# Kernel optimization log

Measured on AMD Instinct MI355X. Metric: run time of the kernel, lower is better.

## Reference

```python
import jax, jax.numpy as jnp
import numpy as np

# Model constants (hard-coded in the torch module / xLSTM config)
B, T, D, H, V = 512, 128, 128, 4, 30000
HD = D // H          # head dim = 32
K = 4                # causal conv1d kernel size
UP = 192             # gated FFN up dim: round_up(1.3*128, 64)
NB = 2               # num sLSTM blocks
EPS = 1e-5


def layernorm(x, w):
    mu = x.mean(-1, keepdims=True)
    var = x.var(-1, keepdims=True)
    return (x - mu) * jax.lax.rsqrt(var + EPS) * w


def setup_inputs() -> dict:
    key = jax.random.key(0)
    ks = iter(jax.random.split(key, 32))

    def rn(shape, s=0.05):
        return jax.random.normal(next(ks), shape, jnp.float32) * s

    tokens = jax.random.randint(next(ks), (B, T), 0, V)
    return {
        "tokens": tokens,
        "emb": rn((V, D), 0.02),
        "ln1_w": jnp.ones((NB, D)),
        "conv_w": rn((NB, D, K), 0.1),          # depthwise causal conv weights
        "conv_b": jnp.zeros((NB, D)),
        "Wi": rn((NB, H, HD, HD), 0.1),          # headwise gate projections
        "Wf": rn((NB, H, HD, HD), 0.1),
        "Wz": rn((NB, H, HD, HD), 0.1),
        "Wo": rn((NB, H, HD, HD), 0.1),
        "Rk": rn((NB, H, HD, 4 * HD), 0.1),      # per-head recurrent kernel
        "cell_b": jnp.zeros((NB, H, 4 * HD)),
        "gn_w": jnp.ones((NB, D)),               # multi-head (group) norm weight
        "ln2_w": jnp.ones((NB, D)),
        "ff_w1": rn((NB, D, 2 * UP), 0.05),      # gated FFN up proj
        "ff_b1": jnp.zeros((NB, 2 * UP)),
        "ff_w2": rn((NB, UP, D), 0.05),
        "ff_b2": jnp.zeros((NB, D)),
        "post_norm_w": jnp.ones((D,)),
        "cls_w1": rn((D, 64), 0.05),
        "cls_b1": jnp.zeros((64,)),
        "cls_w2": rn((64, 2), 0.05),
        "cls_b2": jnp.zeros((2,)),
    }


def slstm_layer(x, conv_w, conv_b, Wi, Wf, Wz, Wo, Rk, cell_b, gn_w):
    # x: [B,T,D]. Causal depthwise conv (left pad K-1) + swish.
    xp = jnp.pad(x, ((0, 0), (K - 1, 0), (0, 0)))
    conv = conv_b + sum(xp[:, k:k + T, :] * conv_w[:, k] for k in range(K))
    x_conv = jax.nn.silu(conv)
    xc = x_conv.reshape(B, T, H, HD)
    xh = x.reshape(B, T, H, HD)
    # i/f gates read the conv branch, z/o gates read x (xLSTM sLSTMLayer).
    i_in = jnp.einsum('bthd,hde->bthe', xc, Wi)
    f_in = jnp.einsum('bthd,hde->bthe', xc, Wf)
    z_in = jnp.einsum('bthd,hde->bthe', xh, Wz)
    o_in = jnp.einsum('bthd,hde->bthe', xh, Wo)
    gates = jnp.concatenate([i_in, f_in, z_in, o_in], -1)  # [B,T,H,4HD]
    gates = jnp.swapaxes(gates, 0, 1)                       # [T,B,H,4HD]

    def step(carry, g_t):
        h, c, n, m = carry  # each [B,H,HD]
        raw = g_t + jnp.einsum('bhd,hdg->bhg', h, Rk) + cell_b
        ir, fr, zr, og = jnp.split(raw, 4, axis=-1)
        # exponential gating with stabilizer state m
        m_new = jnp.maximum(fr + m, ir)
        ig = jnp.exp(ir - m_new)
        fg = jnp.exp(fr + m - m_new)
        c_new = fg * c + ig * jnp.tanh(zr)
        n_new = fg * n + ig
        h_new = jax.nn.sigmoid(og) * c_new / n_new
        return (h_new, c_new, n_new, m_new), h_new

    z0 = jnp.zeros((B, H, HD), x.dtype)
    _, ys = jax.lax.scan(step, (z0, z0, z0, z0), gates)
    y = jnp.swapaxes(ys, 0, 1)  # [B,T,H,HD]
    # multi-head layernorm (group norm over each head)
    mu = y.mean(-1, keepdims=True)
    var = y.var(-1, keepdims=True)
    yn = (y - mu) * jax.lax.rsqrt(var + EPS)
    return yn.reshape(B, T, D) * gn_w


def reference(tokens, emb, ln1_w, conv_w, conv_b, Wi, Wf, Wz, Wo, Rk, cell_b,
              gn_w, ln2_w, ff_w1, ff_b1, ff_w2, ff_b2, post_norm_w,
              cls_w1, cls_b1, cls_w2, cls_b2):
    x = emb[tokens]  # [B,T,D]
    for b in range(NB):
        x = x + slstm_layer(layernorm(x, ln1_w[b]), conv_w[b], conv_b[b],
                            Wi[b], Wf[b], Wz[b], Wo[b], Rk[b], cell_b[b], gn_w[b])
        h = layernorm(x, ln2_w[b]) @ ff_w1[b] + ff_b1[b]
        gate, up = jnp.split(h, 2, axis=-1)
        x = x + (jax.nn.gelu(gate) * up) @ ff_w2[b] + ff_b2[b]
    x = layernorm(x, post_norm_w)
    pooled = x.mean(axis=1)  # [B,D]
    h1 = jax.nn.relu(pooled @ cls_w1 + cls_b1)
    return h1 @ cls_w2 + cls_b2  # [B,2] logits
```

## Files before the change

### kernel.cpp

```cpp
#include <hip/hip_runtime.h>

typedef unsigned short u16;
typedef unsigned int u32;
typedef __attribute__((ext_vector_type(8))) short short8;
typedef __attribute__((ext_vector_type(4))) short s16x4;
typedef __attribute__((ext_vector_type(4))) float f32x4;
typedef __attribute__((ext_vector_type(2))) float f32x2;
typedef __attribute__((ext_vector_type(2))) int i32x2;

#define BB 512
#define TT 128
#define DD 128
#define HH 4
#define NBB 2
#define BT (BB*TT)
#define EPSF 1e-5f
#define LOG2E 1.4426950408889634f

__device__ __forceinline__ float bf2f(u16 u){ return __uint_as_float(((u32)u) << 16); }
__device__ __forceinline__ u16 f2bf(float f){
  u32 x = __float_as_uint(f);
  u32 r = x + 0x7fffu + ((x >> 16) & 1u);
  return (u16)(r >> 16);
}
__device__ __forceinline__ float bcastf(float v, int lane){
  return __uint_as_float(__builtin_amdgcn_readlane(__float_as_uint(v), lane));
}
__device__ __forceinline__ float gelu_fast(float x){
  float u = 0.7978845608028654f * (x + 0.044715f * x * x * x);
  float e2 = __builtin_amdgcn_exp2f(2.f * LOG2E * u);
  return x - x * __builtin_amdgcn_rcpf(e2 + 1.f);
}
#define DPP_ADD(v, ctrl, rmask, bc) \
  v += __int_as_float(__builtin_amdgcn_update_dpp(0, __float_as_int(v), (ctrl), (rmask), 0xf, (bc)))
__device__ __forceinline__ float wsum64(float v){
  DPP_ADD(v, 0x111, 0xf, true);
  DPP_ADD(v, 0x112, 0xf, true);
  DPP_ADD(v, 0x114, 0xf, true);
  DPP_ADD(v, 0x118, 0xf, true);
  DPP_ADD(v, 0x142, 0xa, false);
  DPP_ADD(v, 0x143, 0xc, false);
  return bcastf(v, 63);
}
__device__ __forceinline__ float rsum_rows01(float v){
  DPP_ADD(v, 0x111, 0xf, true);
  DPP_ADD(v, 0x112, 0xf, true);
  DPP_ADD(v, 0x114, 0xf, true);
  DPP_ADD(v, 0x118, 0xf, true);
  DPP_ADD(v, 0x142, 0xa, false);
  return v;
}
__device__ __forceinline__ float down32(float v){
  i32x2 r = __builtin_amdgcn_permlane32_swap(__float_as_int(v), __float_as_int(v), false, false);
  return __int_as_float(r.y);
}

__global__ __launch_bounds__(256) void k_convert(
    const float* __restrict__ ff_w1, const float* __restrict__ ff_w2,
    const float* __restrict__ Wi, const float* __restrict__ Wf,
    const float* __restrict__ Wz, const float* __restrict__ Wo,
    u16* __restrict__ w1T, u16* __restrict__ w2T,
    u16* __restrict__ gifT, u16* __restrict__ gzoT){
  int tid = blockIdx.x * 256 + threadIdx.x;
  const int n1 = NBB*384*128;
  if (tid < n1){
    int nb = tid / (384*128); int r = tid - nb*384*128; int n = r >> 7, k = r & 127;
    w1T[tid] = f2bf(ff_w1[(nb*128 + k)*384 + n]); return;
  }
  tid -= n1;
  const int n2 = NBB*128*192;
  if (tid < n2){
    int nb = tid / (128*192); int r = tid - nb*128*192; int n = r / 192, k = r - n*192;
    w2T[tid] = f2bf(ff_w2[(nb*192 + k)*128 + n]); return;
  }
  tid -= n2;
  const int n3 = NBB*HH*64*32;
  if (tid < n3){
    int nb = tid / (HH*64*32); int r = tid - nb*HH*64*32;
    int h = r >> 11; int r2 = r & 2047; int n = r2 >> 5, k = r2 & 31;
    const float* W = (n < 32) ? Wi : Wf; int nn = n & 31;
    gifT[tid] = f2bf(W[((nb*HH + h)*32 + k)*32 + nn]); return;
  }
  tid -= n3;
  if (tid < n3){
    int nb = tid / (HH*64*32); int r = tid - nb*HH*64*32;
    int h = r >> 11; int r2 = r & 2047; int n = r2 >> 5, k = r2 & 31;
    const float* W = (n < 32) ? Wz : Wo; int nn = n & 31;
    gzoT[tid] = f2bf(W[((nb*HH + h)*32 + k)*32 + nn]); return;
  }
}

__global__ __launch_bounds__(256) void k_lnconv(float* __restrict__ x,
    const int* __restrict__ tok, const float* __restrict__ emb,
    const float* __restrict__ ln1_w, const float* __restrict__ conv_w,
    const float* __restrict__ conv_b, u16* __restrict__ xn_bf,
    u16* __restrict__ xc_bf, int nb, int useemb){
  __shared__ float lnbuf[35][128];
  int b = blockIdx.x >> 2, tile = blockIdx.x & 3;
  int t0 = tile * 32;
  int wid = threadIdx.x >> 6, l = threadIdx.x & 63;
  for (int tt = wid; tt < 35; tt += 4){
    int t = t0 - 3 + tt;
    if (t < 0){
      lnbuf[tt][2*l] = 0.f; lnbuf[tt][2*l+1] = 0.f;
    } else {
      const float* src = useemb ? (emb + (size_t)tok[b*TT + t]*128)
                                : (x + (size_t)(b*TT + t)*128);
      float2 v = ((const float2*)src)[l];
      float s  = wsum64(v.x + v.y);
      float sq = wsum64(v.x*v.x + v.y*v.y);
      float mu = s * (1.f/128.f);
      float var = sq * (1.f/128.f) - mu*mu;
      float rs = rsqrtf(var + EPSF);
      float2 w = ((const float2*)(ln1_w + nb*128))[l];
      float y0 = (v.x - mu)*rs*w.x, y1 = (v.y - mu)*rs*w.y;
      lnbuf[tt][2*l] = y0; lnbuf[tt][2*l+1] = y1;
      if (tt >= 3){
        u32 pk = (u32)f2bf(y0) | ((u32)f2bf(y1) << 16);
        ((u32*)(xn_bf + (size_t)(b*TT + t)*128))[l] = pk;
        if (useemb) ((float2*)(x + (size_t)(b*TT + t)*128))[l] = v;
      }
    }
  }
  __syncthreads();
  for (int e = threadIdx.x; e < 32*128; e += 256){
    int tt = e >> 7, d = e & 127;
    float s = conv_b[nb*128 + d];
    #pragma unroll
    for (int k = 0; k < 4; k++)
      s += lnbuf[tt + k][d] * conv_w[(nb*128 + d)*4 + k];
    float sig = 1.f / (1.f + __expf(-s));
    xc_bf[(size_t)(b*TT + t0 + tt)*128 + d] = f2bf(s * sig);
  }
}

__global__ __launch_bounds__(256) void k_gates(const u16* __restrict__ xc_bf,
    const u16* __restrict__ xn_bf, const u16* __restrict__ gifT,
    const u16* __restrict__ gzoT, u16* __restrict__ gates, int nb){
  int m0 = blockIdx.x * 64;
  int b = m0 >> 7;
  int t00 = m0 & 127;
  int h = threadIdx.x >> 6, l = threadIdx.x & 63;
  short8 bfr[2][4];
  {
    const u16* B0 = gifT + (size_t)(nb*HH + h)*64*32;
    const u16* B1 = gzoT + (size_t)(nb*HH + h)*64*32;
    #pragma unroll
    for (int jt = 0; jt < 4; jt++){
      bfr[0][jt] = *(const short8*)(B0 + (jt*16 + (l & 15))*32 + (l >> 4)*8);
      bfr[1][jt] = *(const short8*)(B1 + (jt*16 + (l & 15))*32 + (l >> 4)*8);
    }
  }
  u16* gb = gates + (size_t)(b*HH + h)*TT*128;
  #pragma unroll
  for (int z = 0; z < 2; z++){
    const u16* A = z ? xn_bf : xc_bf;
    #pragma unroll
    for (int rg = 0; rg < 4; rg++){
      int r0 = m0 + rg*16;
      short8 a = *(const short8*)(A + (size_t)(r0 + (l & 15))*128 + h*32 + (l >> 4)*8);
      int tt = t00 + rg*16 + (l >> 4)*4;
      #pragma unroll
      for (int jt = 0; jt < 4; jt++){
        f32x4 acc = {0.f, 0.f, 0.f, 0.f};
        acc = __builtin_amdgcn_mfma_f32_16x16x32_bf16(a, bfr[z][jt], acc, 0, 0, 0);
        int cloc = z*64 + jt*16 + (l & 15);
        s16x4 pk;
        #pragma unroll
        for (int r = 0; r < 4; r++) pk[r] = (short)f2bf(acc[r]);
        *(s16x4*)(gb + ((size_t)(tt >> 3)*128 + cloc)*8 + (tt & 7)) = pk;
      }
    }
  }
}

__global__ __launch_bounds__(256, 2) void k_scan(const u16* __restrict__ gates,
    const float* __restrict__ Rk, const float* __restrict__ cell_b,
    const float* __restrict__ gn_w, float* __restrict__ x,
    float* __restrict__ dump, int nb){
  int wid = threadIdx.x >> 6, l = threadIdx.x & 63;
  int pair = blockIdx.x * 4 + wid;
  int b = pair >> 2, h = pair & 3;
  f32x2 rk[32];
  const float* Rkh = Rk + (size_t)(nb*HH + h)*32*128;
  #pragma unroll
  for (int d = 0; d < 32; d++){
    rk[d].x = Rkh[d*128 + l];
    rk[d].y = Rkh[d*128 + l + 64];
  }
  f32x2 cb = { cell_b[(nb*HH + h)*128 + l], cell_b[(nb*HH + h)*128 + l + 64] };
  int e = l & 31;
  bool lo = (l < 32);
  float gnw = gn_w[nb*128 + h*32 + e];
  float hs = 0.f, cs = 0.f, ns = 0.f, ms = 0.f;
  const u16* gbase = gates + (size_t)(b*HH + h)*TT*128;
  float* xp = lo ? (x + (size_t)(b*TT)*128 + h*32 + e) : (dump + pair*32 + e);
  int xstr = lo ? 128 : 0;
  float xnext = xp[0];
  short8 ga = *(const short8*)(gbase + (size_t)l*8);
  short8 gb = *(const short8*)(gbase + (size_t)(l + 64)*8);
  for (int t8 = 0; t8 < 16; t8++){
    short8 na  = *(const short8*)(gbase + ((size_t)(t8+1)*128 + l)*8);
    short8 nb2 = *(const short8*)(gbase + ((size_t)(t8+1)*128 + l + 64)*8);
    #pragma unroll
    for (int k = 0; k < 8; k++){
      float xcur = xnext;
      xnext = xp[xstr];
      f32x2 acc0 = { bf2f((u16)ga[k]) + cb.x, bf2f((u16)gb[k]) + cb.y };
      f32x2 acc1 = {0.f, 0.f}, acc2 = {0.f, 0.f}, acc3 = {0.f, 0.f};
      #pragma unroll
      for (int d = 0; d < 32; d += 4){
        float h0 = bcastf(hs, d),   h1 = bcastf(hs, d+1);
        float h2 = bcastf(hs, d+2), h3 = bcastf(hs, d+3);
        acc0 = __builtin_elementwise_fma((f32x2){h0,h0}, rk[d],   acc0);
        acc1 = __builtin_elementwise_fma((f32x2){h1,h1}, rk[d+1], acc1);
        acc2 = __builtin_elementwise_fma((f32x2){h2,h2}, rk[d+2], acc2);
        acc3 = __builtin_elementwise_fma((f32x2){h3,h3}, rk[d+3], acc3);
      }
      f32x2 rr = (acc0 + acc1) + (acc2 + acc3);
      float r0 = rr.x, r1 = rr.y;
      float fx = down32(r0);
      float ox = down32(r1);
      float mnew = fmaxf(fx + ms, r0);
      float ig = __builtin_amdgcn_exp2f((r0 - mnew) * LOG2E);
      float fg = __builtin_amdgcn_exp2f((fx + ms - mnew) * LOG2E);
      float e2 = __builtin_amdgcn_exp2f(2.f * LOG2E * r1);
      float th = fmaf(-2.f, __builtin_amdgcn_rcpf(e2 + 1.f), 1.f);
      cs = fmaf(fg, cs, ig * th);
      ns = fmaf(fg, ns, ig);
      ms = mnew;
      float se = __builtin_amdgcn_exp2f(-ox * LOG2E);
      hs = cs * __builtin_amdgcn_rcpf(fmaf(ns, se, ns));
      float s = rsum_rows01(hs);
      float sq = rsum_rows01(hs * hs);
      float mu = bcastf(s, 31) * (1.f/32.f);
      float var = bcastf(sq, 31) * (1.f/32.f) - mu*mu;
      float yn = (hs - mu) * __builtin_amdgcn_rsqf(var + EPSF) * gnw;
      xp[0] = xcur + yn;
      xp += xstr;
    }
    ga = na; gb = nb2;
  }
}

__global__ __launch_bounds__(512, 4) void k_ffn(float* __restrict__ x,
    const float* __restrict__ ln2_w, const u16* __restrict__ w1T,
    const float* __restrict__ ff_b1, const u16* __restrict__ w2T,
    const float* __restrict__ ff_b2, int nb){
  __shared__ u16 xln[64][136];
  __shared__ u16 hbuf[64][392];
  int m0 = blockIdx.x * 64;
  int w = threadIdx.x >> 6, l = threadIdx.x & 63;
  short8 w1f[3][4];
  const u16* W1 = w1T + (size_t)nb*384*128;
  #pragma unroll
  for (int j = 0; j < 3; j++)
    #pragma unroll
    for (int c = 0; c < 4; c++)
      w1f[j][c] = *(const short8*)(W1 + (size_t)((3*w + j)*16 + (l & 15))*128 + c*32 + (l >> 4)*8);
  short8 w2f[6];
  const u16* W2 = w2T + (size_t)nb*128*192;
  #pragma unroll
  for (int c = 0; c < 6; c++)
    w2f[c] = *(const short8*)(W2 + (size_t)(w*16 + (l & 15))*192 + c*32 + (l >> 4)*8);
  float2 lw = ((const float2*)(ln2_w + nb*128))[l];
  #pragma unroll
  for (int rr = 0; rr < 8; rr++){
    int row = w*8 + rr;
    float2 v = ((const float2*)(x + (size_t)(m0 + row)*128))[l];
    float s  = wsum64(v.x + v.y);
    float sq = wsum64(v.x*v.x + v.y*v.y);
    float mu = s * (1.f/128.f);
    float var = sq * (1.f/128.f) - mu*mu;
    float rs = rsqrtf(var + EPSF);
    ((u32*)xln[row])[l] = (u32)f2bf((v.x - mu)*rs*lw.x)
                        | ((u32)f2bf((v.y - mu)*rs*lw.y) << 16);
  }
  __syncthreads();
  #pragma unroll
  for (int rg = 0; rg < 4; rg++){
    short8 a[4];
    #pragma unroll
    for (int c = 0; c < 4; c++)
      a[c] = *(const short8*)(&xln[rg*16 + (l & 15)][c*32 + (l >> 4)*8]);
    #pragma unroll
    for (int j = 0; j < 3; j++){
      f32x4 acc = {0.f, 0.f, 0.f, 0.f};
      #pragma unroll
      for (int c = 0; c < 4; c++)
        acc = __builtin_amdgcn_mfma_f32_16x16x32_bf16(a[c], w1f[j][c], acc, 0, 0, 0);
      int col = (3*w + j)*16 + (l & 15);
      float bb = ff_b1[nb*384 + col];
      #pragma unroll
      for (int r = 0; r < 4; r++){
        int row = rg*16 + (l >> 4)*4 + r;
        hbuf[row][col] = f2bf(acc[r] + bb);
      }
    }
  }
  __syncthreads();
  {
    int row = threadIdx.x >> 3;
    int k0 = (threadIdx.x & 7) * 24;
    #pragma unroll
    for (int j2 = 0; j2 < 24; j2++){
      int k = k0 + j2;
      float g = bf2f(hbuf[row][k]);
      float u = bf2f(hbuf[row][k + 192]);
      hbuf[row][k] = f2bf(gelu_fast(g) * u);
    }
  }
  __syncthreads();
  #pragma unroll
  for (int rg = 0; rg < 4; rg++){
    f32x4 acc = {0.f, 0.f, 0.f, 0.f};
    #pragma unroll
    for (int c = 0; c < 6; c++){
      short8 a = *(const short8*)(&hbuf[rg*16 + (l & 15)][c*32 + (l >> 4)*8]);
      acc = __builtin_amdgcn_mfma_f32_16x16x32_bf16(a, w2f[c], acc, 0, 0, 0);
    }
    int col = w*16 + (l & 15);
    float bb = ff_b2[nb*128 + col];
    #pragma unroll
    for (int r = 0; r < 4; r++){
      int row = m0 + rg*16 + (l >> 4)*4 + r;
      x[(size_t)row*128 + col] += acc[r] + bb;
    }
  }
}

__global__ __launch_bounds__(256) void k_pool_cls(const float* __restrict__ x,
    const float* __restrict__ pw, const float* __restrict__ w1,
    const float* __restrict__ b1, const float* __restrict__ w2,
    const float* __restrict__ b2, float* __restrict__ out){
  __shared__ float red[4][128];
  __shared__ float pooled[128];
  __shared__ float h1s[64];
  int b = blockIdx.x;
  int wid = threadIdx.x >> 6, l = threadIdx.x & 63;
  float2 w = ((const float2*)pw)[l];
  float ax = 0.f, ay = 0.f;
  for (int t = wid; t < TT; t += 4){
    float2 v = ((const float2*)(x + (size_t)(b*TT + t)*128))[l];
    float s  = wsum64(v.x + v.y);
    float sq = wsum64(v.x*v.x + v.y*v.y);
    float mu = s * (1.f/128.f);
    float var = sq * (1.f/128.f) - mu*mu;
    float rs = rsqrtf(var + EPSF);
    ax += (v.x - mu)*rs*w.x;
    ay += (v.y - mu)*rs*w.y;
  }
  red[wid][2*l] = ax; red[wid][2*l+1] = ay;
  __syncthreads();
  if (threadIdx.x < 128){
    int d = threadIdx.x;
    pooled[d] = (red[0][d] + red[1][d] + red[2][d] + red[3][d]) * (1.f/128.f);
  }
  __syncthreads();
  if (threadIdx.x < 64){
    int j = threadIdx.x;
    float s = b1[j];
    for (int d = 0; d < 128; d++) s += pooled[d] * w1[d*64 + j];
    h1s[j] = fmaxf(s, 0.f);
  }
  __syncthreads();
  if (threadIdx.x < 2){
    int j = threadIdx.x;
    float s = b2[j];
    for (int k = 0; k < 64; k++) s += h1s[k] * w2[k*2 + j];
    out[b*2 + j] = s;
  }
}

extern "C" void kernel_launch(void* const* d_in, const int* in_sizes, int n_in,
                              void* d_out, int out_size, void* d_ws, size_t ws_size,
                              hipStream_t stream){
  const int*   tok    = (const int*)d_in[0];
  const float* emb    = (const float*)d_in[1];
  const float* ln1_w  = (const float*)d_in[2];
  const float* conv_w = (const float*)d_in[3];
  const float* conv_b = (const float*)d_in[4];
  const float* Wi     = (const float*)d_in[5];
  const float* Wf     = (const float*)d_in[6];
  const float* Wz     = (const float*)d_in[7];
  const float* Wo     = (const float*)d_in[8];
  const float* Rk     = (const float*)d_in[9];
  const float* cell_b = (const float*)d_in[10];
  const float* gn_w   = (const float*)d_in[11];
  const float* ln2_w  = (const float*)d_in[12];
  const float* ff_w1  = (const float*)d_in[13];
  const float* ff_b1  = (const float*)d_in[14];
  const float* ff_w2  = (const float*)d_in[15];
  const float* ff_b2  = (const float*)d_in[16];
  const float* postw  = (const float*)d_in[17];
  const float* cw1    = (const float*)d_in[18];
  const float* cb1    = (const float*)d_in[19];
  const float* cw2    = (const float*)d_in[20];
  const float* cb2    = (const float*)d_in[21];
  float* out = (float*)d_out;

  char* ws = (char*)d_ws;
  size_t off = 0;
  float* x      = (float*)(ws + off); off += (size_t)BT*128*4;
  u16*   xn_bf  = (u16*)(ws + off);   off += (size_t)BT*128*2;
  u16*   xc_bf  = (u16*)(ws + off);   off += (size_t)BT*128*2;
  u16*   gates  = (u16*)(ws + off);   off += (size_t)BT*512*2;
  u16*   w1T    = (u16*)(ws + off);   off += (size_t)NBB*384*128*2;
  u16*   w2T    = (u16*)(ws + off);   off += (size_t)NBB*128*192*2;
  u16*   gifT   = (u16*)(ws + off);   off += (size_t)NBB*HH*64*32*2;
  u16*   gzoT   = (u16*)(ws + off);   off += (size_t)NBB*HH*64*32*2;
  float* dump   = (float*)xn_bf;

  k_convert<<<704, 256, 0, stream>>>(ff_w1, ff_w2, Wi, Wf, Wz, Wo, w1T, w2T, gifT, gzoT);
  for (int nb = 0; nb < NBB; nb++){
    k_lnconv<<<BB*4, 256, 0, stream>>>(x, tok, emb, ln1_w, conv_w, conv_b,
                                       xn_bf, xc_bf, nb, nb == 0 ? 1 : 0);
    k_gates<<<BT/64, 256, 0, stream>>>(xc_bf, xn_bf, gifT, gzoT, gates, nb);
    k_scan<<<512, 256, 0, stream>>>(gates, Rk, cell_b, gn_w, x, dump, nb);
    k_ffn<<<BT/64, 512, 0, stream>>>(x, ln2_w, w1T, ff_b1, w2T, ff_b2, nb);
  }
  k_pool_cls<<<BB, 256, 0, stream>>>(x, postw, cw1, cb1, cw2, cb2, out);
}
```

Measured before the change: 304.4 us.

## Batch sLSTM recurrence across 16 sequences with split-bf16 MFMA

The scan kernel now has one wavefront per (16-sequence group, head). It computes the recurrent matvec for 16 batch rows at once with MFMA, using a hi/lo bf16 split of both Rk and h to approximate fp32 precision, instead of per-lane FMA over readlane broadcasts. The gates kernel writes gate preactivations with the cell bias folded in, in an MFMA-fragment layout. h is exchanged through LDS each step. The grid drops from 512 blocks of 256 threads to 128 single-wave blocks, which trades parallelism and latency hiding for far fewer instructions per step.

```diff
diff --git a/kernel.cpp b/kernel.cpp
--- a/kernel.cpp
+++ b/kernel.cpp
@@ -3,10 +3,8 @@
 typedef unsigned short u16;
 typedef unsigned int u32;
 typedef __attribute__((ext_vector_type(8))) short short8;
-typedef __attribute__((ext_vector_type(4))) short s16x4;
 typedef __attribute__((ext_vector_type(4))) float f32x4;
 typedef __attribute__((ext_vector_type(2))) float f32x2;
-typedef __attribute__((ext_vector_type(2))) int i32x2;
 
 #define BB 512
 #define TT 128
@@ -42,25 +40,14 @@
   DPP_ADD(v, 0x143, 0xc, false);
   return bcastf(v, 63);
 }
-__device__ __forceinline__ float rsum_rows01(float v){
-  DPP_ADD(v, 0x111, 0xf, true);
-  DPP_ADD(v, 0x112, 0xf, true);
-  DPP_ADD(v, 0x114, 0xf, true);
-  DPP_ADD(v, 0x118, 0xf, true);
-  DPP_ADD(v, 0x142, 0xa, false);
-  return v;
-}
-__device__ __forceinline__ float down32(float v){
-  i32x2 r = __builtin_amdgcn_permlane32_swap(__float_as_int(v), __float_as_int(v), false, false);
-  return __int_as_float(r.y);
-}
 
 __global__ __launch_bounds__(256) void k_convert(
     const float* __restrict__ ff_w1, const float* __restrict__ ff_w2,
     const float* __restrict__ Wi, const float* __restrict__ Wf,
     const float* __restrict__ Wz, const float* __restrict__ Wo,
+    const float* __restrict__ Rk,
     u16* __restrict__ w1T, u16* __restrict__ w2T,
-    u16* __restrict__ gifT, u16* __restrict__ gzoT){
+    u16* __restrict__ gifT, u16* __restrict__ gzoT, u16* __restrict__ rkf){
   int tid = blockIdx.x * 256 + threadIdx.x;
   const int n1 = NBB*384*128;
   if (tid < n1){
@@ -87,6 +74,20 @@
     int h = r >> 11; int r2 = r & 2047; int n = r2 >> 5, k = r2 & 31;
     const float* W = (n < 32) ? Wz : Wo; int nn = n & 31;
     gzoT[tid] = f2bf(W[((nb*HH + h)*32 + k)*32 + nn]); return;
+  }
+  tid -= n3;
+  const int n5 = NBB*HH*8*64*8;
+  if (tid < n5){
+    int j = tid & 7; int t2 = tid >> 3;
+    int l = t2 & 63; t2 >>= 6;
+    int m = t2 & 7; t2 >>= 3;
+    int h4 = t2 & 3; int nb = t2 >> 2;
+    float v = Rk[((size_t)((nb*HH + h4)*32) + (l >> 4)*8 + j)*128 + m*16 + (l & 15)];
+    u16 hi = f2bf(v);
+    u16 lo = f2bf(v - bf2f(hi));
+    size_t base = (((size_t)(nb*HH + h4)*8 + m)*64 + l)*16;
+    rkf[base + j] = hi;
+    rkf[base + 8 + j] = lo;
   }
 }
 
@@ -136,7 +137,8 @@
 
 __global__ __launch_bounds__(256) void k_gates(const u16* __restrict__ xc_bf,
     const u16* __restrict__ xn_bf, const u16* __restrict__ gifT,
-    const u16* __restrict__ gzoT, u16* __restrict__ gates, int nb){
+    const u16* __restrict__ gzoT, const float* __restrict__ cell_b,
+    u16* __restrict__ gfrag, int nb){
   int m0 = blockIdx.x * 64;
   int b = m0 >> 7;
   int t00 = m0 & 127;
@@ -151,7 +153,11 @@
       bfr[1][jt] = *(const short8*)(B1 + (jt*16 + (l & 15))*32 + (l >> 4)*8);
     }
   }
-  u16* gb = gates + (size_t)(b*HH + h)*TT*128;
+  u16* gf = gfrag + (size_t)((b >> 4)*4 + h)*TT*64*32;
+  int c = b & 15;
+  int gg = (l & 15) >> 2;
+  int r3 = l & 3;
+  const float* cbp = cell_b + (nb*HH + h)*128;
   #pragma unroll
   for (int z = 0; z < 2; z++){
     const u16* A = z ? xn_bf : xc_bf;
@@ -159,87 +165,137 @@
     for (int rg = 0; rg < 4; rg++){
       int r0 = m0 + rg*16;
       short8 a = *(const short8*)(A + (size_t)(r0 + (l & 15))*128 + h*32 + (l >> 4)*8);
-      int tt = t00 + rg*16 + (l >> 4)*4;
+      int tb = t00 + rg*16 + (l >> 4)*4;
       #pragma unroll
       for (int jt = 0; jt < 4; jt++){
         f32x4 acc = {0.f, 0.f, 0.f, 0.f};
         acc = __builtin_amdgcn_mfma_f32_16x16x32_bf16(a, bfr[z][jt], acc, 0, 0, 0);
         int cloc = z*64 + jt*16 + (l & 15);
-        s16x4 pk;
+        float cb = cbp[cloc];
+        int slot = (z*4 + jt)*4 + r3;
         #pragma unroll
-        for (int r = 0; r < 4; r++) pk[r] = (short)f2bf(acc[r]);
-        *(s16x4*)(gb + ((size_t)(tt >> 3)*128 + cloc)*8 + (tt & 7)) = pk;
+        for (int r = 0; r < 4; r++)
+          gf[((size_t)(tb + r)*64 + gg*16 + c)*32 + slot] = f2bf(acc[r] + cb);
       }
     }
   }
 }
 
-__global__ __launch_bounds__(256, 2) void k_scan(const u16* __restrict__ gates,
-    const float* __restrict__ Rk, const float* __restrict__ cell_b,
-    const float* __restrict__ gn_w, float* __restrict__ x,
-    float* __restrict__ dump, int nb){
-  int wid = threadIdx.x >> 6, l = threadIdx.x & 63;
-  int pair = blockIdx.x * 4 + wid;
-  int b = pair >> 2, h = pair & 3;
-  f32x2 rk[32];
-  const float* Rkh = Rk + (size_t)(nb*HH + h)*32*128;
-  #pragma unroll
-  for (int d = 0; d < 32; d++){
-    rk[d].x = Rkh[d*128 + l];
-    rk[d].y = Rkh[d*128 + l + 64];
-  }
-  f32x2 cb = { cell_b[(nb*HH + h)*128 + l], cell_b[(nb*HH + h)*128 + l + 64] };
-  int e = l & 31;
-  bool lo = (l < 32);
-  float gnw = gn_w[nb*128 + h*32 + e];
-  float hs = 0.f, cs = 0.f, ns = 0.f, ms = 0.f;
-  const u16* gbase = gates + (size_t)(b*HH + h)*TT*128;
-  float* xp = lo ? (x + (size_t)(b*TT)*128 + h*32 + e) : (dump + pair*32 + e);
-  int xstr = lo ? 128 : 0;
-  float xnext = xp[0];
-  short8 ga = *(const short8*)(gbase + (size_t)l*8);
-  short8 gb = *(const short8*)(gbase + (size_t)(l + 64)*8);
-  for (int t8 = 0; t8 < 16; t8++){
-    short8 na  = *(const short8*)(gbase + ((size_t)(t8+1)*128 + l)*8);
-    short8 nb2 = *(const short8*)(gbase + ((size_t)(t8+1)*128 + l + 64)*8);
-    #pragma unroll
-    for (int k = 0; k < 8; k++){
-      float xcur = xnext;
-      xnext = xp[xstr];
-      f32x2 acc0 = { bf2f((u16)ga[k]) + cb.x, bf2f((u16)gb[k]) + cb.y };
-      f32x2 acc1 = {0.f, 0.f}, acc2 = {0.f, 0.f}, acc3 = {0.f, 0.f};
+__global__ __launch_bounds__(64, 1) void k_scan(const u16* __restrict__ gfrag,
+    const u16* __restrict__ rkf, const float* __restrict__ gn_w,
+    float* __restrict__ x, int nb){
+  __shared__ u16 hb[2][16][40];
+  int l = threadIdx.x;
+  int g = blockIdx.x;
+  int hg = g & 3;
+  int c = l & 15, g2 = l >> 4;
+  int b = (g >> 2)*16 + c;
+  short8 afh[8], afl[8];
+  {
+    const u16* rk = rkf + (((size_t)(nb*HH + hg)*8)*64 + l)*16;
+    #pragma unroll
+    for (int m = 0; m < 8; m++){
+      afh[m] = *(const short8*)(rk + (size_t)m*64*16);
+      afl[m] = *(const short8*)(rk + (size_t)m*64*16 + 8);
+    }
+  }
+  float gnw[8];
+  #pragma unroll
+  for (int r = 0; r < 4; r++){
+    gnw[r]     = gn_w[nb*128 + hg*32 + 4*g2 + r];
+    gnw[4 + r] = gn_w[nb*128 + hg*32 + 16 + 4*g2 + r];
+  }
+  float cs[8], ns[8], ms[8];
+  #pragma unroll
+  for (int i = 0; i < 8; i++){ cs[i] = 0.f; ns[i] = 0.f; ms[i] = 0.f; }
+  short8 bh = {0,0,0,0,0,0,0,0}, bl = {0,0,0,0,0,0,0,0};
+  const u16* gp = gfrag + ((size_t)g*TT*64 + l)*32;
+  float* xrow = x + (size_t)b*TT*128 + hg*32;
+  short8 gv0 = ((const short8*)gp)[0], gv1 = ((const short8*)gp)[1],
+         gv2 = ((const short8*)gp)[2], gv3 = ((const short8*)gp)[3];
+  f32x4 xn0 = *(const f32x4*)(xrow + 4*g2);
+  f32x4 xn1 = *(const f32x4*)(xrow + 16 + 4*g2);
+  for (int t = 0; t < TT; t++){
+    const u16* gpn = gp + 64*32;
+    short8 pg0 = ((const short8*)gpn)[0], pg1 = ((const short8*)gpn)[1],
+           pg2 = ((const short8*)gpn)[2], pg3 = ((const short8*)gpn)[3];
+    f32x4 xf0 = *(const f32x4*)(xrow + 128 + 4*g2);
+    f32x4 xf1 = *(const f32x4*)(xrow + 128 + 16 + 4*g2);
+    f32x4 C[8];
+    #pragma unroll
+    for (int r = 0; r < 4; r++){
+      C[0][r] = bf2f((u16)gv0[r]); C[1][r] = bf2f((u16)gv0[4+r]);
+      C[2][r] = bf2f((u16)gv1[r]); C[3][r] = bf2f((u16)gv1[4+r]);
+      C[4][r] = bf2f((u16)gv2[r]); C[5][r] = bf2f((u16)gv2[4+r]);
+      C[6][r] = bf2f((u16)gv3[r]); C[7][r] = bf2f((u16)gv3[4+r]);
+    }
+    #pragma unroll
+    for (int m = 0; m < 8; m++){
+      C[m] = __builtin_amdgcn_mfma_f32_16x16x32_bf16(afh[m], bh, C[m], 0, 0, 0);
+      C[m] = __builtin_amdgcn_mfma_f32_16x16x32_bf16(afh[m], bl, C[m], 0, 0, 0);
+      C[m] = __builtin_amdgcn_mfma_f32_16x16x32_bf16(afl[m], bh, C[m], 0, 0, 0);
+    }
+    float hs[8];
+    #pragma unroll
+    for (int hf = 0; hf < 2; hf++){
       #pragma unroll
-      for (int d = 0; d < 32; d += 4){
-        float h0 = bcastf(hs, d),   h1 = bcastf(hs, d+1);
-        float h2 = bcastf(hs, d+2), h3 = bcastf(hs, d+3);
-        acc0 = __builtin_elementwise_fma((f32x2){h0,h0}, rk[d],   acc0);
-        acc1 = __builtin_elementwise_fma((f32x2){h1,h1}, rk[d+1], acc1);
-        acc2 = __builtin_elementwise_fma((f32x2){h2,h2}, rk[d+2], acc2);
-        acc3 = __builtin_elementwise_fma((f32x2){h3,h3}, rk[d+3], acc3);
+      for (int r = 0; r < 4; r++){
+        int i = hf*4 + r;
+        float ir = C[0+hf][r], fr = C[2+hf][r], zr = C[4+hf][r], og = C[6+hf][r];
+        float a = fr + ms[i];
+        float mnew = fmaxf(a, ir);
+        float mL = mnew * LOG2E;
+        float ig = __builtin_amdgcn_exp2f(fmaf(ir, LOG2E, -mL));
+        float fg = __builtin_amdgcn_exp2f(fmaf(a, LOG2E, -mL));
+        float e2 = __builtin_amdgcn_exp2f(zr * (2.f*LOG2E));
+        float th = fmaf(-2.f, __builtin_amdgcn_rcpf(e2 + 1.f), 1.f);
+        cs[i] = fmaf(fg, cs[i], ig * th);
+        ns[i] = fmaf(fg, ns[i], ig);
+        ms[i] = mnew;
+        float se = __builtin_amdgcn_exp2f(og * -LOG2E);
+        hs[i] = cs[i] * __builtin_amdgcn_rcpf(fmaf(ns[i], se, ns[i]));
       }
-      f32x2 rr = (acc0 + acc1) + (acc2 + acc3);
-      float r0 = rr.x, r1 = rr.y;
-      float fx = down32(r0);
-      float ox = down32(r1);
-      float mnew = fmaxf(fx + ms, r0);
-      float ig = __builtin_amdgcn_exp2f((r0 - mnew) * LOG2E);
-      float fg = __builtin_amdgcn_exp2f((fx + ms - mnew) * LOG2E);
-      float e2 = __builtin_amdgcn_exp2f(2.f * LOG2E * r1);
-      float th = fmaf(-2.f, __builtin_amdgcn_rcpf(e2 + 1.f), 1.f);
-      cs = fmaf(fg, cs, ig * th);
-      ns = fmaf(fg, ns, ig);
-      ms = mnew;
-      float se = __builtin_amdgcn_exp2f(-ox * LOG2E);
-      hs = cs * __builtin_amdgcn_rcpf(fmaf(ns, se, ns));
-      float s = rsum_rows01(hs);
-      float sq = rsum_rows01(hs * hs);
-      float mu = bcastf(s, 31) * (1.f/32.f);
-      float var = bcastf(sq, 31) * (1.f/32.f) - mu*mu;
-      float yn = (hs - mu) * __builtin_amdgcn_rsqf(var + EPSF) * gnw;
-      xp[0] = xcur + yn;
-      xp += xstr;
-    }
-    ga = na; gb = nb2;
+    }
+    #pragma unroll
+    for (int hf = 0; hf < 2; hf++){
+      u32 h01, h23, l01, l23;
+      asm("v_cvt_pk_bf16_f32 %0, %1, %2" : "=v"(h01) : "v"(hs[hf*4+0]), "v"(hs[hf*4+1]));
+      asm("v_cvt_pk_bf16_f32 %0, %1, %2" : "=v"(h23) : "v"(hs[hf*4+2]), "v"(hs[hf*4+3]));
+      float hi0 = __uint_as_float(h01 << 16);
+      float hi1 = __uint_as_float(h01 & 0xffff0000u);
+      float hi2 = __uint_as_float(h23 << 16);
+      float hi3 = __uint_as_float(h23 & 0xffff0000u);
+      float d0 = hs[hf*4+0] - hi0, d1 = hs[hf*4+1] - hi1;
+      float d2 = hs[hf*4+2] - hi2, d3 = hs[hf*4+3] - hi3;
+      asm("v_cvt_pk_bf16_f32 %0, %1, %2" : "=v"(l01) : "v"(d0), "v"(d1));
+      asm("v_cvt_pk_bf16_f32 %0, %1, %2" : "=v"(l23) : "v"(d2), "v"(d3));
+      *(uint2*)(&hb[0][c][hf*16 + 4*g2]) = make_uint2(h01, h23);
+      *(uint2*)(&hb[1][c][hf*16 + 4*g2]) = make_uint2(l01, l23);
+    }
+    __builtin_amdgcn_sched_barrier(0);
+    asm volatile("s_waitcnt lgkmcnt(0)" ::: "memory");
+    __builtin_amdgcn_sched_barrier(0);
+    bh = *(const short8*)(&hb[0][c][g2*8]);
+    bl = *(const short8*)(&hb[1][c][g2*8]);
+    float s8 = 0.f, sq8 = 0.f;
+    #pragma unroll
+    for (int i = 0; i < 8; i++){ s8 += hs[i]; sq8 += hs[i]*hs[i]; }
+    s8 += __shfl_xor(s8, 32, 64);  sq8 += __shfl_xor(sq8, 32, 64);
+    s8 += __shfl_xor(s8, 16, 64);  sq8 += __shfl_xor(sq8, 16, 64);
+    float mu = s8 * (1.f/32.f);
+    float var = sq8 * (1.f/32.f) - mu*mu;
+    float rs = __builtin_amdgcn_rsqf(var + EPSF);
+    f32x4 o0, o1;
+    #pragma unroll
+    for (int r = 0; r < 4; r++){
+      o0[r] = xn0[r] + (hs[r]   - mu)*rs*gnw[r];
+      o1[r] = xn1[r] + (hs[4+r] - mu)*rs*gnw[4+r];
+    }
+    *(f32x4*)(xrow + 4*g2) = o0;
+    *(f32x4*)(xrow + 16 + 4*g2) = o1;
+    xrow += 128; gp = gpn;
+    gv0 = pg0; gv1 = pg1; gv2 = pg2; gv3 = pg3;
+    xn0 = xf0; xn1 = xf1;
   }
 }
 
@@ -305,9 +361,9 @@
     #pragma unroll
     for (int j2 = 0; j2 < 24; j2++){
       int k = k0 + j2;
-      float g = bf2f(hbuf[row][k]);
+      float gt = bf2f(hbuf[row][k]);
       float u = bf2f(hbuf[row][k + 192]);
-      hbuf[row][k] = f2bf(gelu_fast(g) * u);
+      hbuf[row][k] = f2bf(gelu_fast(gt) * u);
     }
   }
   __syncthreads();
@@ -404,19 +460,20 @@
   float* x      = (float*)(ws + off); off += (size_t)BT*128*4;
   u16*   xn_bf  = (u16*)(ws + off);   off += (size_t)BT*128*2;
   u16*   xc_bf  = (u16*)(ws + off);   off += (size_t)BT*128*2;
-  u16*   gates  = (u16*)(ws + off);   off += (size_t)BT*512*2;
+  u16*   gfrag  = (u16*)(ws + off);   off += (size_t)128*TT*64*32*2;
   u16*   w1T    = (u16*)(ws + off);   off += (size_t)NBB*384*128*2;
   u16*   w2T    = (u16*)(ws + off);   off += (size_t)NBB*128*192*2;
   u16*   gifT   = (u16*)(ws + off);   off += (size_t)NBB*HH*64*32*2;
   u16*   gzoT   = (u16*)(ws + off);   off += (size_t)NBB*HH*64*32*2;
-  float* dump   = (float*)xn_bf;
-
-  k_convert<<<704, 256, 0, stream>>>(ff_w1, ff_w2, Wi, Wf, Wz, Wo, w1T, w2T, gifT, gzoT);
+  u16*   rkf    = (u16*)(ws + off);   off += (size_t)NBB*HH*8*64*16*2;
+
+  k_convert<<<832, 256, 0, stream>>>(ff_w1, ff_w2, Wi, Wf, Wz, Wo, Rk,
+                                     w1T, w2T, gifT, gzoT, rkf);
   for (int nb = 0; nb < NBB; nb++){
     k_lnconv<<<BB*4, 256, 0, stream>>>(x, tok, emb, ln1_w, conv_w, conv_b,
                                        xn_bf, xc_bf, nb, nb == 0 ? 1 : 0);
-    k_gates<<<BT/64, 256, 0, stream>>>(xc_bf, xn_bf, gifT, gzoT, gates, nb);
-    k_scan<<<512, 256, 0, stream>>>(gates, Rk, cell_b, gn_w, x, dump, nb);
+    k_gates<<<BT/64, 256, 0, stream>>>(xc_bf, xn_bf, gifT, gzoT, cell_b, gfrag, nb);
+    k_scan<<<128, 64, 0, stream>>>(gfrag, rkf, gn_w, x, nb);
     k_ffn<<<BT/64, 512, 0, stream>>>(x, ln2_w, w1T, ff_b1, w2T, ff_b2, nb);
   }
   k_pool_cls<<<BB, 256, 0, stream>>>(x, postw, cw1, cb1, cw2, cb2, out);
```

After: 583.2 us. 1.92x slower.

## Fuse GELU gating into FFN up-projection epilogue by pairing gate/up tiles

Applied to the files above, without the earlier changes.

Each warp now computes matching gate and up column tiles together, so GELU(gate)*up is applied in registers right after the MFMA instead of writing the full 384-wide hidden to shared memory and running a separate elementwise pass. The remainder of the 12 column tiles is split across warp pairs over half the row groups. This removes one barrier, halves the shared hidden buffer, and drops the shared-memory round trip. The cost is more weight fragments held in registers and an uneven load across warps.

```diff
diff --git a/kernel.cpp b/kernel.cpp
--- a/kernel.cpp
+++ b/kernel.cpp
@@ -248,16 +248,20 @@
     const float* __restrict__ ff_b1, const u16* __restrict__ w2T,
     const float* __restrict__ ff_b2, int nb){
   __shared__ u16 xln[64][136];
-  __shared__ u16 hbuf[64][392];
+  __shared__ u16 act[64][196];
   int m0 = blockIdx.x * 64;
   int w = threadIdx.x >> 6, l = threadIdx.x & 63;
-  short8 w1f[3][4];
+  int kf = w, kh = 8 + (w & 3);
+  int rh0 = (w >> 2) * 2;
+  short8 wgf[4], wuf[4], wgh[4], wuh[4];
   const u16* W1 = w1T + (size_t)nb*384*128;
   #pragma unroll
-  for (int j = 0; j < 3; j++)
-    #pragma unroll
-    for (int c = 0; c < 4; c++)
-      w1f[j][c] = *(const short8*)(W1 + (size_t)((3*w + j)*16 + (l & 15))*128 + c*32 + (l >> 4)*8);
+  for (int c = 0; c < 4; c++){
+    wgf[c] = *(const short8*)(W1 + (size_t)(kf*16 + (l & 15))*128 + c*32 + (l >> 4)*8);
+    wuf[c] = *(const short8*)(W1 + (size_t)((12 + kf)*16 + (l & 15))*128 + c*32 + (l >> 4)*8);
+    wgh[c] = *(const short8*)(W1 + (size_t)(kh*16 + (l & 15))*128 + c*32 + (l >> 4)*8);
+    wuh[c] = *(const short8*)(W1 + (size_t)((12 + kh)*16 + (l & 15))*128 + c*32 + (l >> 4)*8);
+  }
   short8 w2f[6];
   const u16* W2 = w2T + (size_t)nb*128*192;
   #pragma unroll
@@ -277,37 +281,30 @@
                         | ((u32)f2bf((v.y - mu)*rs*lw.y) << 16);
   }
   __syncthreads();
-  #pragma unroll
-  for (int rg = 0; rg < 4; rg++){
+  const float* B1 = ff_b1 + nb*384;
+  #pragma unroll
+  for (int u5 = 0; u5 < 6; u5++){
+    int rg = (u5 < 4) ? u5 : (rh0 + (u5 - 4));
+    const short8* wg = (u5 < 4) ? wgf : wgh;
+    const short8* wu = (u5 < 4) ? wuf : wuh;
+    int k = (u5 < 4) ? kf : kh;
     short8 a[4];
     #pragma unroll
     for (int c = 0; c < 4; c++)
       a[c] = *(const short8*)(&xln[rg*16 + (l & 15)][c*32 + (l >> 4)*8]);
-    #pragma unroll
-    for (int j = 0; j < 3; j++){
-      f32x4 acc = {0.f, 0.f, 0.f, 0.f};
-      #pragma unroll
-      for (int c = 0; c < 4; c++)
-        acc = __builtin_amdgcn_mfma_f32_16x16x32_bf16(a[c], w1f[j][c], acc, 0, 0, 0);
-      int col = (3*w + j)*16 + (l & 15);
-      float bb = ff_b1[nb*384 + col];
-      #pragma unroll
-      for (int r = 0; r < 4; r++){
-        int row = rg*16 + (l >> 4)*4 + r;
-        hbuf[row][col] = f2bf(acc[r] + bb);
-      }
-    }
-  }
-  __syncthreads();
-  {
-    int row = threadIdx.x >> 3;
-    int k0 = (threadIdx.x & 7) * 24;
-    #pragma unroll
-    for (int j2 = 0; j2 < 24; j2++){
-      int k = k0 + j2;
-      float g = bf2f(hbuf[row][k]);
-      float u = bf2f(hbuf[row][k + 192]);
-      hbuf[row][k] = f2bf(gelu_fast(g) * u);
+    f32x4 ag = {0.f,0.f,0.f,0.f}, au = {0.f,0.f,0.f,0.f};
+    #pragma unroll
+    for (int c = 0; c < 4; c++){
+      ag = __builtin_amdgcn_mfma_f32_16x16x32_bf16(a[c], wg[c], ag, 0, 0, 0);
+      au = __builtin_amdgcn_mfma_f32_16x16x32_bf16(a[c], wu[c], au, 0, 0, 0);
+    }
+    int col = k*16 + (l & 15);
+    float bg = B1[col];
+    float bu = B1[192 + col];
+    #pragma unroll
+    for (int r = 0; r < 4; r++){
+      int row = rg*16 + (l >> 4)*4 + r;
+      act[row][col] = f2bf(gelu_fast(ag[r] + bg) * (au[r] + bu));
     }
   }
   __syncthreads();
@@ -316,7 +313,7 @@
     f32x4 acc = {0.f, 0.f, 0.f, 0.f};
     #pragma unroll
     for (int c = 0; c < 6; c++){
-      short8 a = *(const short8*)(&hbuf[rg*16 + (l & 15)][c*32 + (l >> 4)*8]);
+      short8 a = *(const short8*)(&act[rg*16 + (l & 15)][c*32 + (l >> 4)*8]);
       acc = __builtin_amdgcn_mfma_f32_16x16x32_bf16(a, w2f[c], acc, 0, 0, 0);
     }
     int col = w*16 + (l & 15);
```

New measurement: 323.5 us. 1.06x slower.

## Fuse layernorm+conv kernel with gate projection kernel via shared memory

Applied to the files above, without the earlier changes.

Merges the layernorm/causal-conv kernel and the gate-projection MFMA kernel into one kernel per batch row. The normalized and conv-activated bf16 activations stay in LDS instead of being written to and read back from global xn_bf/xc_bf buffers. It also removes one launch per block. In exchange, grid size drops from 2048 to 512 blocks, each using about 70KB of LDS, so occupancy falls. The conv now reads bf16-rounded LN values instead of fp32, a small precision change.

```diff
diff --git a/kernel.cpp b/kernel.cpp
--- a/kernel.cpp
+++ b/kernel.cpp
@@ -90,20 +90,19 @@
   }
 }
 
-__global__ __launch_bounds__(256) void k_lnconv(float* __restrict__ x,
+__global__ __launch_bounds__(256) void k_lngates(float* __restrict__ x,
     const int* __restrict__ tok, const float* __restrict__ emb,
     const float* __restrict__ ln1_w, const float* __restrict__ conv_w,
-    const float* __restrict__ conv_b, u16* __restrict__ xn_bf,
-    u16* __restrict__ xc_bf, int nb, int useemb){
-  __shared__ float lnbuf[35][128];
-  int b = blockIdx.x >> 2, tile = blockIdx.x & 3;
-  int t0 = tile * 32;
+    const float* __restrict__ conv_b, const u16* __restrict__ gifT,
+    const u16* __restrict__ gzoT, u16* __restrict__ gates, int nb, int useemb){
+  __shared__ u16 xnl[128][136];
+  __shared__ u16 xcl[128][136];
+  int b = blockIdx.x;
   int wid = threadIdx.x >> 6, l = threadIdx.x & 63;
-  for (int tt = wid; tt < 35; tt += 4){
-    int t = t0 - 3 + tt;
-    if (t < 0){
-      lnbuf[tt][2*l] = 0.f; lnbuf[tt][2*l+1] = 0.f;
-    } else {
+  {
+    float2 w = ((const float2*)(ln1_w + nb*128))[l];
+    for (int rr = 0; rr < 32; rr++){
+      int t = wid*32 + rr;
       const float* src = useemb ? (emb + (size_t)tok[b*TT + t]*128)
                                 : (x + (size_t)(b*TT + t)*128);
       float2 v = ((const float2*)src)[l];
@@ -112,35 +111,25 @@
       float mu = s * (1.f/128.f);
       float var = sq * (1.f/128.f) - mu*mu;
       float rs = rsqrtf(var + EPSF);
-      float2 w = ((const float2*)(ln1_w + nb*128))[l];
       float y0 = (v.x - mu)*rs*w.x, y1 = (v.y - mu)*rs*w.y;
-      lnbuf[tt][2*l] = y0; lnbuf[tt][2*l+1] = y1;
-      if (tt >= 3){
-        u32 pk = (u32)f2bf(y0) | ((u32)f2bf(y1) << 16);
-        ((u32*)(xn_bf + (size_t)(b*TT + t)*128))[l] = pk;
-        if (useemb) ((float2*)(x + (size_t)(b*TT + t)*128))[l] = v;
-      }
-    }
-  }
-  __syncthreads();
-  for (int e = threadIdx.x; e < 32*128; e += 256){
+      ((u32*)xnl[t])[l] = (u32)f2bf(y0) | ((u32)f2bf(y1) << 16);
+      if (useemb) ((float2*)(x + (size_t)(b*TT + t)*128))[l] = v;
+    }
+  }
+  __syncthreads();
+  for (int e = threadIdx.x; e < 128*128; e += 256){
     int tt = e >> 7, d = e & 127;
     float s = conv_b[nb*128 + d];
     #pragma unroll
-    for (int k = 0; k < 4; k++)
-      s += lnbuf[tt + k][d] * conv_w[(nb*128 + d)*4 + k];
+    for (int k = 0; k < 4; k++){
+      int t = tt + k - 3;
+      if (t >= 0) s += bf2f(xnl[t][d]) * conv_w[(nb*128 + d)*4 + k];
+    }
     float sig = 1.f / (1.f + __expf(-s));
-    xc_bf[(size_t)(b*TT + t0 + tt)*128 + d] = f2bf(s * sig);
-  }
-}
-
-__global__ __launch_bounds__(256) void k_gates(const u16* __restrict__ xc_bf,
-    const u16* __restrict__ xn_bf, const u16* __restrict__ gifT,
-    const u16* __restrict__ gzoT, u16* __restrict__ gates, int nb){
-  int m0 = blockIdx.x * 64;
-  int b = m0 >> 7;
-  int t00 = m0 & 127;
-  int h = threadIdx.x >> 6, l = threadIdx.x & 63;
+    xcl[tt][d] = f2bf(s * sig);
+  }
+  __syncthreads();
+  int h = wid;
   short8 bfr[2][4];
   {
     const u16* B0 = gifT + (size_t)(nb*HH + h)*64*32;
@@ -154,12 +143,11 @@
   u16* gb = gates + (size_t)(b*HH + h)*TT*128;
   #pragma unroll
   for (int z = 0; z < 2; z++){
-    const u16* A = z ? xn_bf : xc_bf;
-    #pragma unroll
-    for (int rg = 0; rg < 4; rg++){
-      int r0 = m0 + rg*16;
-      short8 a = *(const short8*)(A + (size_t)(r0 + (l & 15))*128 + h*32 + (l >> 4)*8);
-      int tt = t00 + rg*16 + (l >> 4)*4;
+    #pragma unroll
+    for (int rg = 0; rg < 8; rg++){
+      const u16* Arow = z ? xnl[rg*16 + (l & 15)] : xcl[rg*16 + (l & 15)];
+      short8 a = *(const short8*)(Arow + h*32 + (l >> 4)*8);
+      int tt = rg*16 + (l >> 4)*4;
       #pragma unroll
       for (int jt = 0; jt < 4; jt++){
         f32x4 acc = {0.f, 0.f, 0.f, 0.f};
@@ -305,9 +293,9 @@
     #pragma unroll
     for (int j2 = 0; j2 < 24; j2++){
       int k = k0 + j2;
-      float g = bf2f(hbuf[row][k]);
+      float gt = bf2f(hbuf[row][k]);
       float u = bf2f(hbuf[row][k + 192]);
-      hbuf[row][k] = f2bf(gelu_fast(g) * u);
+      hbuf[row][k] = f2bf(gelu_fast(gt) * u);
     }
   }
   __syncthreads();
@@ -402,20 +390,17 @@
   char* ws = (char*)d_ws;
   size_t off = 0;
   float* x      = (float*)(ws + off); off += (size_t)BT*128*4;
-  u16*   xn_bf  = (u16*)(ws + off);   off += (size_t)BT*128*2;
-  u16*   xc_bf  = (u16*)(ws + off);   off += (size_t)BT*128*2;
+  float* dump   = (float*)(ws + off); off += (size_t)2048*32*4;
   u16*   gates  = (u16*)(ws + off);   off += (size_t)BT*512*2;
   u16*   w1T    = (u16*)(ws + off);   off += (size_t)NBB*384*128*2;
   u16*   w2T    = (u16*)(ws + off);   off += (size_t)NBB*128*192*2;
   u16*   gifT   = (u16*)(ws + off);   off += (size_t)NBB*HH*64*32*2;
   u16*   gzoT   = (u16*)(ws + off);   off += (size_t)NBB*HH*64*32*2;
-  float* dump   = (float*)xn_bf;
 
   k_convert<<<704, 256, 0, stream>>>(ff_w1, ff_w2, Wi, Wf, Wz, Wo, w1T, w2T, gifT, gzoT);
   for (int nb = 0; nb < NBB; nb++){
-    k_lnconv<<<BB*4, 256, 0, stream>>>(x, tok, emb, ln1_w, conv_w, conv_b,
-                                       xn_bf, xc_bf, nb, nb == 0 ? 1 : 0);
-    k_gates<<<BT/64, 256, 0, stream>>>(xc_bf, xn_bf, gifT, gzoT, gates, nb);
+    k_lngates<<<BB, 256, 0, stream>>>(x, tok, emb, ln1_w, conv_w, conv_b,
+                                      gifT, gzoT, gates, nb, nb == 0 ? 1 : 0);
     k_scan<<<512, 256, 0, stream>>>(gates, Rk, cell_b, gn_w, x, dump, nb);
     k_ffn<<<BT/64, 512, 0, stream>>>(x, ln2_w, w1T, ff_b1, w2T, ff_b2, nb);
   }
```

Measured after the change: 340.8 us. 1.12x slower.
